# Optimization experiments

Hardware: AMD Instinct MI355X
Metric: run time of the kernel (lower is better)

Reference implementation:

```python
import jax, jax.numpy as jnp
import numpy as np

N_NODES = 50000
N_EDGES = 800000


def gat_layer(x, src, dst, W, al, ar, b, activation):
    # x: [N, F_in], W: [F_in, H*D], al/ar: [H, D], b: [H*D]
    H, D = al.shape
    n = x.shape[0]
    h = (x @ W).reshape(n, H, D)                      # [N, H, D]
    el = jnp.sum(h * al, axis=-1)                     # [N, H]
    er = jnp.sum(h * ar, axis=-1)                     # [N, H]
    e = jax.nn.leaky_relu(el[src] + er[dst], 0.2)     # [E, H]
    # segment softmax over incoming edges of each dst node
    m = jax.ops.segment_max(e, dst, num_segments=n)   # [N, H]
    ex = jnp.exp(e - m[dst])                          # [E, H]
    s = jax.ops.segment_sum(ex, dst, num_segments=n)  # [N, H]
    a = ex / s[dst]                                   # [E, H]
    msg = h[src] * a[:, :, None]                      # [E, H, D]
    out = jax.ops.segment_sum(msg, dst, num_segments=n) + b.reshape(1, H, D)
    return activation(out) if activation is not None else out


def setup_inputs() -> dict:
    key = jax.random.key(0)
    ks = jax.random.split(key, 12)
    feat = jax.random.normal(ks[0], (N_NODES, 128), dtype=jnp.float32)
    src = jax.random.randint(ks[1], (N_EDGES,), 0, N_NODES)
    dst = jax.random.randint(ks[2], (N_EDGES,), 0, N_NODES)
    sc = 0.1
    return {
        "feat": feat, "src": src, "dst": dst,
        "W1": jax.random.normal(ks[3], (128, 256), jnp.float32) * sc,
        "al1": jax.random.normal(ks[4], (4, 64), jnp.float32) * sc,
        "ar1": jax.random.normal(ks[5], (4, 64), jnp.float32) * sc,
        "b1": jnp.zeros((256,), jnp.float32),
        "W2": jax.random.normal(ks[6], (256, 256), jnp.float32) * sc,
        "al2": jax.random.normal(ks[7], (4, 64), jnp.float32) * sc,
        "ar2": jax.random.normal(ks[8], (4, 64), jnp.float32) * sc,
        "b2": jnp.zeros((256,), jnp.float32),
        "W3": jax.random.normal(ks[9], (256, 8), jnp.float32) * sc,
        "al3": jax.random.normal(ks[10], (1, 8), jnp.float32) * sc,
        "ar3": jax.random.normal(ks[11], (1, 8), jnp.float32) * sc,
        "b3": jnp.zeros((8,), jnp.float32),
    }


def reference(feat, src, dst, W1, al1, ar1, b1, W2, al2, ar2, b2, W3, al3, ar3, b3):
    n = feat.shape[0]
    elu = jax.nn.elu
    h = gat_layer(feat, src, dst, W1, al1, ar1, b1, elu).reshape(n, -1)  # flatten heads
    h = gat_layer(h, src, dst, W2, al2, ar2, b2, elu).reshape(n, -1)
    h = gat_layer(h, src, dst, W3, al3, ar3, b3, None)                   # [N, 1, out]
    return h.mean(axis=1)                                               # head mean -> [N, out]
```

## Files before the change

kernel.cpp:

```cpp
#include <hip/hip_runtime.h>
#include <math.h>


typedef _Float16 half8 __attribute__((ext_vector_type(8)));
typedef _Float16 half4 __attribute__((ext_vector_type(4)));
typedef float    floatx4 __attribute__((ext_vector_type(4)));

__device__ __forceinline__ float leaky02(float x) { return x > 0.f ? x : 0.2f * x; }

__global__ void count_edges(const int* __restrict__ dst, int* __restrict__ cnt, int E) {
    int i = blockIdx.x * blockDim.x + threadIdx.x;
    if (i < E) atomicAdd(&cnt[dst[i]], 1);
}

__global__ void scan_block(const int* __restrict__ cnt, int* __restrict__ incl,
                           int* __restrict__ bsum, int n) {
    __shared__ int sh[256];
    int tid = threadIdx.x;
    int i = blockIdx.x * 256 + tid;
    int v = (i < n) ? cnt[i] : 0;
    sh[tid] = v;
    __syncthreads();
    for (int o = 1; o < 256; o <<= 1) {
        int t = (tid >= o) ? sh[tid - o] : 0;
        __syncthreads();
        sh[tid] += t;
        __syncthreads();
    }
    if (i < n) incl[i] = sh[tid];
    if (tid == 255) bsum[blockIdx.x] = sh[255];
}

__global__ void scan_sums(int* __restrict__ bsum, int g) {
    __shared__ int sh[256];
    int tid = threadIdx.x;
    int v = (tid < g) ? bsum[tid] : 0;
    sh[tid] = v;
    __syncthreads();
    for (int o = 1; o < 256; o <<= 1) {
        int t = (tid >= o) ? sh[tid - o] : 0;
        __syncthreads();
        sh[tid] += t;
        __syncthreads();
    }
    if (tid < g) bsum[tid] = sh[tid] - v;
}

__global__ void finalize_rowptr(const int* __restrict__ incl, const int* __restrict__ cnt,
                                const int* __restrict__ bsum, int* __restrict__ row_ptr,
                                int* __restrict__ nxt, int n, int E) {
    int i = blockIdx.x * 256 + threadIdx.x;
    if (i < n) {
        int v = incl[i] - cnt[i] + bsum[blockIdx.x];
        row_ptr[i] = v;
        nxt[i] = v;
    }
    if (i == 0) row_ptr[n] = E;
}

__global__ void fill_csr(const int* __restrict__ src, const int* __restrict__ dst,
                         int* __restrict__ nxt, int* __restrict__ csr_src, int E) {
    int i = blockIdx.x * blockDim.x + threadIdx.x;
    if (i < E) {
        int p = atomicAdd(&nxt[dst[i]], 1);
        csr_src[p] = src[i];
    }
}

__global__ void transpose_w2(const float* __restrict__ W1, _Float16* __restrict__ W1T,
                             const float* __restrict__ W2, _Float16* __restrict__ W2T) {
    int i = blockIdx.x * 256 + threadIdx.x;
    if (i < 128 * 256) {
        int m = i >> 7, k = i & 127;
        W1T[i] = (_Float16)W1[k * 256 + m];
    } else {
        int j = i - 128 * 256;
        if (j < 256 * 256) {
            int m = j >> 8, k = j & 255;
            W2T[j] = (_Float16)W2[k * 256 + m];
        }
    }
}

#define GBM 128
#define GBK 32

template <bool AF32>
__global__ __launch_bounds__(256)
void gemm_mfma(const void* __restrict__ Ap, const _Float16* __restrict__ BT,
               _Float16* __restrict__ C, int N, int K) {
    __shared__ _Float16 As[GBM][GBK + 8];
    __shared__ _Float16 Bs[GBM][GBK + 8];
    int tid  = threadIdx.x;
    int wave = tid >> 6, lane = tid & 63;
    int quad = lane >> 4, l16 = lane & 15;
    int row0 = blockIdx.y * GBM;
    int col0 = blockIdx.x * GBM;

    floatx4 acc[8][2];
    #pragma unroll
    for (int i = 0; i < 8; ++i)
        #pragma unroll
        for (int j = 0; j < 2; ++j)
            #pragma unroll
            for (int e = 0; e < 4; ++e) acc[i][j][e] = 0.f;

    for (int k0 = 0; k0 < K; k0 += GBK) {
        if (AF32) {
            const float* Af = (const float*)Ap;
            #pragma unroll
            for (int it = 0; it < 4; ++it) {
                int s = it * 256 + tid;
                int r = s >> 3, off = (s & 7) * 4;
                float4 v = make_float4(0.f, 0.f, 0.f, 0.f);
                int gr = row0 + r;
                if (gr < N) v = *(const float4*)&Af[(size_t)gr * K + k0 + off];
                half4 hv;
                hv[0] = (_Float16)v.x; hv[1] = (_Float16)v.y;
                hv[2] = (_Float16)v.z; hv[3] = (_Float16)v.w;
                *(half4*)&As[r][off] = hv;
            }
        } else {
            const _Float16* Ah = (const _Float16*)Ap;
            #pragma unroll
            for (int it = 0; it < 2; ++it) {
                int s = it * 256 + tid;
                int r = s >> 2, off = (s & 3) * 8;
                half8 v;
                #pragma unroll
                for (int q = 0; q < 8; ++q) v[q] = (_Float16)0.f;
                int gr = row0 + r;
                if (gr < N) v = *(const half8*)&Ah[(size_t)gr * K + k0 + off];
                *(half8*)&As[r][off] = v;
            }
        }
        #pragma unroll
        for (int it = 0; it < 2; ++it) {
            int s = it * 256 + tid;
            int r = s >> 2, off = (s & 3) * 8;
            half8 w = *(const half8*)&BT[(size_t)(col0 + r) * K + k0 + off];
            *(half8*)&Bs[r][off] = w;
        }
        __syncthreads();
        half8 bfrag[2];
        #pragma unroll
        for (int ct = 0; ct < 2; ++ct)
            bfrag[ct] = *(const half8*)&Bs[wave * 32 + ct * 16 + l16][quad * 8];
        #pragma unroll
        for (int rt = 0; rt < 8; ++rt) {
            half8 afrag = *(const half8*)&As[rt * 16 + l16][quad * 8];
            acc[rt][0] = __builtin_amdgcn_mfma_f32_16x16x32_f16(afrag, bfrag[0], acc[rt][0], 0, 0, 0);
            acc[rt][1] = __builtin_amdgcn_mfma_f32_16x16x32_f16(afrag, bfrag[1], acc[rt][1], 0, 0, 0);
        }
        __syncthreads();
    }
    #pragma unroll
    for (int rt = 0; rt < 8; ++rt) {
        #pragma unroll
        for (int reg = 0; reg < 4; ++reg) {
            int gr = row0 + rt * 16 + quad * 4 + reg;
            if (gr < N) {
                #pragma unroll
                for (int ct = 0; ct < 2; ++ct) {
                    int gc = col0 + wave * 32 + ct * 16 + l16;
                    C[(size_t)gr * 256 + gc] = (_Float16)acc[rt][ct][reg];
                }
            }
        }
    }
}

__global__ __launch_bounds__(256)
void attn_lr(const _Float16* __restrict__ h16, const float* __restrict__ al,
             const float* __restrict__ ar, float* __restrict__ el,
             float* __restrict__ er, int NH) {
    int wid = (blockIdx.x * 256 + threadIdx.x) >> 6;
    int lane = threadIdx.x & 63;
    int r = lane >> 3, c = lane & 7;
    int row = wid * 8 + r;
    if (row >= NH) return;
    int hd = row & 3;
    half8 hv = *(const half8*)&h16[(size_t)row * 64 + c * 8];
    const float* alp = &al[hd * 64 + c * 8];
    const float* arp = &ar[hd * 64 + c * 8];
    float l = 0.f, rr = 0.f;
    #pragma unroll
    for (int q = 0; q < 8; ++q) {
        float v = (float)hv[q];
        l  += v * alp[q];
        rr += v * arp[q];
    }
    l  += __shfl_xor(l, 1);  l  += __shfl_xor(l, 2);  l  += __shfl_xor(l, 4);
    rr += __shfl_xor(rr, 1); rr += __shfl_xor(rr, 2); rr += __shfl_xor(rr, 4);
    if (c == 0) { el[row] = l; er[row] = rr; }
}

__global__ __launch_bounds__(256)
void gat_agg(const _Float16* __restrict__ h16, const float* __restrict__ el,
             const float* __restrict__ er, const int* __restrict__ row_ptr,
             const int* __restrict__ csr_src, const float* __restrict__ bias,
             _Float16* __restrict__ out, int N) {
    int tid = threadIdx.x;
    int l32 = tid & 31;
    int node = blockIdx.x * 8 + (tid >> 5);
    if (node >= N) return;
    int beg = row_ptr[node], end = row_ptr[node + 1];
    int deg = end - beg;
    int hd = l32 >> 3;

    float er0 = er[node * 4 + 0], er1 = er[node * 4 + 1];
    float er2 = er[node * 4 + 2], er3 = er[node * 4 + 3];

    float m0, m1, m2, m3, s0, s1, s2, s3;
    if (deg <= 32) {
        float e0 = -INFINITY, e1 = -INFINITY, e2 = -INFINITY, e3 = -INFINITY;
        bool act = l32 < deg;
        if (act) {
            int sv = csr_src[beg + l32];
            e0 = leaky02(el[sv * 4 + 0] + er0);
            e1 = leaky02(el[sv * 4 + 1] + er1);
            e2 = leaky02(el[sv * 4 + 2] + er2);
            e3 = leaky02(el[sv * 4 + 3] + er3);
        }
        m0 = e0; m1 = e1; m2 = e2; m3 = e3;
        #pragma unroll
        for (int msk = 1; msk < 32; msk <<= 1) {
            m0 = fmaxf(m0, __shfl_xor(m0, msk));
            m1 = fmaxf(m1, __shfl_xor(m1, msk));
            m2 = fmaxf(m2, __shfl_xor(m2, msk));
            m3 = fmaxf(m3, __shfl_xor(m3, msk));
        }
        s0 = act ? __expf(e0 - m0) : 0.f;
        s1 = act ? __expf(e1 - m1) : 0.f;
        s2 = act ? __expf(e2 - m2) : 0.f;
        s3 = act ? __expf(e3 - m3) : 0.f;
        #pragma unroll
        for (int msk = 1; msk < 32; msk <<= 1) {
            s0 += __shfl_xor(s0, msk);
            s1 += __shfl_xor(s1, msk);
            s2 += __shfl_xor(s2, msk);
            s3 += __shfl_xor(s3, msk);
        }
    } else {
        m0 = m1 = m2 = m3 = -INFINITY;
        for (int j = beg + l32; j < end; j += 32) {
            int sv = csr_src[j];
            m0 = fmaxf(m0, leaky02(el[sv * 4 + 0] + er0));
            m1 = fmaxf(m1, leaky02(el[sv * 4 + 1] + er1));
            m2 = fmaxf(m2, leaky02(el[sv * 4 + 2] + er2));
            m3 = fmaxf(m3, leaky02(el[sv * 4 + 3] + er3));
        }
        #pragma unroll
        for (int msk = 1; msk < 32; msk <<= 1) {
            m0 = fmaxf(m0, __shfl_xor(m0, msk));
            m1 = fmaxf(m1, __shfl_xor(m1, msk));
            m2 = fmaxf(m2, __shfl_xor(m2, msk));
            m3 = fmaxf(m3, __shfl_xor(m3, msk));
        }
        s0 = s1 = s2 = s3 = 0.f;
        for (int j = beg + l32; j < end; j += 32) {
            int sv = csr_src[j];
            s0 += __expf(leaky02(el[sv * 4 + 0] + er0) - m0);
            s1 += __expf(leaky02(el[sv * 4 + 1] + er1) - m1);
            s2 += __expf(leaky02(el[sv * 4 + 2] + er2) - m2);
            s3 += __expf(leaky02(el[sv * 4 + 3] + er3) - m3);
        }
        #pragma unroll
        for (int msk = 1; msk < 32; msk <<= 1) {
            s0 += __shfl_xor(s0, msk);
            s1 += __shfl_xor(s1, msk);
            s2 += __shfl_xor(s2, msk);
            s3 += __shfl_xor(s3, msk);
        }
    }
    float mh  = (hd & 2) ? ((hd & 1) ? m3 : m2) : ((hd & 1) ? m1 : m0);
    float sh_ = (hd & 2) ? ((hd & 1) ? s3 : s2) : ((hd & 1) ? s1 : s0);
    float erh = (hd & 2) ? ((hd & 1) ? er3 : er2) : ((hd & 1) ? er1 : er0);
    float ih  = sh_ > 0.f ? 1.f / sh_ : 0.f;

    const _Float16* hb = h16 + l32 * 8;
    float acc[8] = {};
    int j = beg;
    for (; j + 4 <= end; j += 4) {
        int sa = csr_src[j], sb = csr_src[j + 1], sc = csr_src[j + 2], sd = csr_src[j + 3];
        float wa = __expf(leaky02(el[sa * 4 + hd] + erh) - mh) * ih;
        float wb = __expf(leaky02(el[sb * 4 + hd] + erh) - mh) * ih;
        float wc = __expf(leaky02(el[sc * 4 + hd] + erh) - mh) * ih;
        float wd = __expf(leaky02(el[sd * 4 + hd] + erh) - mh) * ih;
        half8 va = *(const half8*)&hb[(size_t)sa * 256];
        half8 vb = *(const half8*)&hb[(size_t)sb * 256];
        half8 vc = *(const half8*)&hb[(size_t)sc * 256];
        half8 vd = *(const half8*)&hb[(size_t)sd * 256];
        #pragma unroll
        for (int q = 0; q < 8; ++q)
            acc[q] += wa * (float)va[q] + wb * (float)vb[q]
                    + wc * (float)vc[q] + wd * (float)vd[q];
    }
    for (; j < end; ++j) {
        int sv = csr_src[j];
        float w = __expf(leaky02(el[sv * 4 + hd] + erh) - mh) * ih;
        half8 v = *(const half8*)&hb[(size_t)sv * 256];
        #pragma unroll
        for (int q = 0; q < 8; ++q) acc[q] += w * (float)v[q];
    }
    half8 o;
    #pragma unroll
    for (int q = 0; q < 8; ++q) {
        float v = acc[q] + bias[l32 * 8 + q];
        v = v > 0.f ? v : (__expf(v) - 1.f);
        o[q] = (_Float16)v;
    }
    *(half8*)&out[(size_t)node * 256 + l32 * 8] = o;
}

__global__ __launch_bounds__(256)
void gemm3_attn(const _Float16* __restrict__ x, const float* __restrict__ W,
                const float* __restrict__ al, const float* __restrict__ ar,
                float* __restrict__ h3, float* __restrict__ el,
                float* __restrict__ er, int N) {
    __shared__ float Ws[256][9];
    int tid = threadIdx.x;
    #pragma unroll
    for (int d = 0; d < 8; ++d) Ws[tid][d] = W[tid * 8 + d];
    __syncthreads();
    int lane = tid & 63;
    int n = blockIdx.x * 4 + (tid >> 6);
    if (n >= N) return;
    float acc[8] = {};
    #pragma unroll
    for (int i = 0; i < 4; ++i) {
        int k = i * 64 + lane;
        float xv = (float)x[(size_t)n * 256 + k];
        #pragma unroll
        for (int d = 0; d < 8; ++d) acc[d] += xv * Ws[k][d];
    }
    #pragma unroll
    for (int d = 0; d < 8; ++d) {
        #pragma unroll
        for (int o = 32; o; o >>= 1) acc[d] += __shfl_down(acc[d], o);
    }
    if (lane == 0) {
        float l = 0.f, r = 0.f;
        #pragma unroll
        for (int d = 0; d < 8; ++d) {
            h3[n * 8 + d] = acc[d];
            l += acc[d] * al[d];
            r += acc[d] * ar[d];
        }
        el[n] = l;
        er[n] = r;
    }
}

__global__ __launch_bounds__(256)
void gat_agg3(const float* __restrict__ h3, const float* __restrict__ el,
              const float* __restrict__ er, const int* __restrict__ row_ptr,
              const int* __restrict__ csr_src, const float* __restrict__ bias,
              float* __restrict__ out, int N) {
    int tid = threadIdx.x;
    int lane = tid & 63;
    int n = blockIdx.x * 4 + (tid >> 6);
    if (n >= N) return;
    int beg = row_ptr[n], end = row_ptr[n + 1];
    float er_n = er[n];
    float mx = -INFINITY;
    for (int j = beg + lane; j < end; j += 64) {
        float e = leaky02(el[csr_src[j]] + er_n);
        mx = fmaxf(mx, e);
    }
    #pragma unroll
    for (int o = 1; o < 64; o <<= 1) mx = fmaxf(mx, __shfl_xor(mx, o));
    float sm = 0.f;
    for (int j = beg + lane; j < end; j += 64) {
        float e = leaky02(el[csr_src[j]] + er_n);
        sm += __expf(e - mx);
    }
    #pragma unroll
    for (int o = 1; o < 64; o <<= 1) sm += __shfl_xor(sm, o);
    float inv = sm > 0.f ? 1.0f / sm : 0.0f;
    int g = lane >> 3, c = lane & 7;
    float acc = 0.f;
    for (int j = beg + g; j < end; j += 8) {
        int s = csr_src[j];
        float a = __expf(leaky02(el[s] + er_n) - mx) * inv;
        acc += h3[s * 8 + c] * a;
    }
    acc += __shfl_xor(acc, 8);
    acc += __shfl_xor(acc, 16);
    acc += __shfl_xor(acc, 32);
    if (lane < 8) out[(size_t)n * 8 + lane] = acc + bias[lane];
}

static inline size_t align_up(size_t x, size_t a) { return (x + a - 1) & ~(a - 1); }

extern "C" void kernel_launch(void* const* d_in, const int* in_sizes, int n_in,
                              void* d_out, int out_size, void* d_ws, size_t ws_size,
                              hipStream_t stream) {
    const float* feat = (const float*)d_in[0];
    const int*   src  = (const int*)d_in[1];
    const int*   dst  = (const int*)d_in[2];
    const float* W1   = (const float*)d_in[3];
    const float* al1  = (const float*)d_in[4];
    const float* ar1  = (const float*)d_in[5];
    const float* b1   = (const float*)d_in[6];
    const float* W2   = (const float*)d_in[7];
    const float* al2  = (const float*)d_in[8];
    const float* ar2  = (const float*)d_in[9];
    const float* b2   = (const float*)d_in[10];
    const float* W3   = (const float*)d_in[11];
    const float* al3  = (const float*)d_in[12];
    const float* ar3  = (const float*)d_in[13];
    const float* b3   = (const float*)d_in[14];

    const int N = in_sizes[0] / 128;
    const int E = in_sizes[1];

    char* w = (char*)d_ws;
    _Float16* bufA16 = (_Float16*)w; w += align_up((size_t)N * 256 * 2, 256);
    _Float16* bufB16 = (_Float16*)w; w += align_up((size_t)N * 256 * 2, 256);
    _Float16* W1T    = (_Float16*)w; w += align_up((size_t)256 * 128 * 2, 256);
    _Float16* W2T    = (_Float16*)w; w += align_up((size_t)256 * 256 * 2, 256);
    float* el      = (float*)w; w += align_up((size_t)N * 4 * 4, 256);
    float* er      = (float*)w; w += align_up((size_t)N * 4 * 4, 256);
    float* h3      = (float*)w; w += align_up((size_t)N * 8 * 4, 256);
    int*   cnt     = (int*)w;   w += align_up((size_t)N * 4, 256);
    int*   incl    = (int*)w;   w += align_up((size_t)N * 4, 256);
    int*   bsum    = (int*)w;   w += align_up(256 * 4, 256);
    int*   row_ptr = (int*)w;   w += align_up(((size_t)N + 1) * 4, 256);
    int*   nxt     = (int*)w;   w += align_up((size_t)N * 4, 256);
    int*   csr_src = (int*)w;   w += align_up((size_t)E * 4, 256);
    (void)ws_size; (void)n_in; (void)out_size;

    const int G1 = (N + 255) / 256;
    const int GE = (E + 255) / 256;

    hipMemsetAsync(cnt, 0, (size_t)N * 4, stream);
    count_edges<<<GE, 256, 0, stream>>>(dst, cnt, E);
    scan_block<<<G1, 256, 0, stream>>>(cnt, incl, bsum, N);
    scan_sums<<<1, 256, 0, stream>>>(bsum, G1);
    finalize_rowptr<<<G1, 256, 0, stream>>>(incl, cnt, bsum, row_ptr, nxt, N, E);
    fill_csr<<<GE, 256, 0, stream>>>(src, dst, nxt, csr_src, E);

    transpose_w2<<<(128 * 256 + 256 * 256 + 255) / 256, 256, 0, stream>>>(W1, W1T, W2, W2T);

    dim3 ggrid(2, (N + GBM - 1) / GBM);
    const int GA = (N + 7) / 8;
    const int GL = (N * 4 + 31) / 32;

    gemm_mfma<true><<<ggrid, 256, 0, stream>>>(feat, W1T, bufA16, N, 128);
    attn_lr<<<GL, 256, 0, stream>>>(bufA16, al1, ar1, el, er, N * 4);
    gat_agg<<<GA, 256, 0, stream>>>(bufA16, el, er, row_ptr, csr_src, b1, bufB16, N);

    gemm_mfma<false><<<ggrid, 256, 0, stream>>>(bufB16, W2T, bufA16, N, 256);
    attn_lr<<<GL, 256, 0, stream>>>(bufA16, al2, ar2, el, er, N * 4);
    gat_agg<<<GA, 256, 0, stream>>>(bufA16, el, er, row_ptr, csr_src, b2, bufB16, N);

    gemm3_attn<<<(N + 3) / 4, 256, 0, stream>>>(bufB16, W3, al3, ar3, h3, el, er, N);
    gat_agg3<<<(N + 3) / 4, 256, 0, stream>>>(h3, el, er, row_ptr, csr_src, b3,
                                              (float*)d_out, N);
}
```

Measured before the change: 433.3 us.

## Fuse attention logits into GEMM epilogue and deepen aggregation gather unroll

Computes el/er attention logits directly from the MFMA accumulators in the GEMM epilogue, using shuffles and shared memory, which removes the separate attn_lr kernel and its reread of h. The scan_sums kernel is dropped and each finalize_rowptr block instead reduces the preceding block sums itself. gat_agg now uses float4 loads for el/er, preloads the bias, and unrolls the gather loop to 8 edges so more loads are in flight. The cost is extra GEMM epilogue work and higher register pressure in the aggregation kernel.

Result: slower. 463.6 us (+7.0%).

```diff
diff --git a/kernel.cpp b/kernel.cpp
--- a/kernel.cpp
+++ b/kernel.cpp
@@ -31,27 +31,23 @@
     if (tid == 255) bsum[blockIdx.x] = sh[255];
 }
 
-__global__ void scan_sums(int* __restrict__ bsum, int g) {
-    __shared__ int sh[256];
-    int tid = threadIdx.x;
-    int v = (tid < g) ? bsum[tid] : 0;
-    sh[tid] = v;
-    __syncthreads();
-    for (int o = 1; o < 256; o <<= 1) {
-        int t = (tid >= o) ? sh[tid - o] : 0;
-        __syncthreads();
-        sh[tid] += t;
-        __syncthreads();
-    }
-    if (tid < g) bsum[tid] = sh[tid] - v;
-}
-
 __global__ void finalize_rowptr(const int* __restrict__ incl, const int* __restrict__ cnt,
                                 const int* __restrict__ bsum, int* __restrict__ row_ptr,
                                 int* __restrict__ nxt, int n, int E) {
-    int i = blockIdx.x * 256 + threadIdx.x;
+    __shared__ int red[256];
+    int bid = blockIdx.x, tid = threadIdx.x;
+    int part = 0;
+    for (int i = tid; i < bid; i += 256) part += bsum[i];
+    red[tid] = part;
+    __syncthreads();
+    for (int o = 128; o; o >>= 1) {
+        if (tid < o) red[tid] += red[tid + o];
+        __syncthreads();
+    }
+    int base = red[0];
+    int i = bid * 256 + tid;
     if (i < n) {
-        int v = incl[i] - cnt[i] + bsum[blockIdx.x];
+        int v = incl[i] - cnt[i] + base;
         row_ptr[i] = v;
         nxt[i] = v;
     }
@@ -88,9 +84,13 @@
 template <bool AF32>
 __global__ __launch_bounds__(256)
 void gemm_mfma(const void* __restrict__ Ap, const _Float16* __restrict__ BT,
-               _Float16* __restrict__ C, int N, int K) {
+               const float* __restrict__ al, const float* __restrict__ ar,
+               _Float16* __restrict__ C, float* __restrict__ el,
+               float* __restrict__ er, int N, int K) {
     __shared__ _Float16 As[GBM][GBK + 8];
     __shared__ _Float16 Bs[GBM][GBK + 8];
+    __shared__ float shEl[4][GBM];
+    __shared__ float shEr[4][GBM];
     int tid  = threadIdx.x;
     int wave = tid >> 6, lane = tid & 63;
     int quad = lane >> 4, l16 = lane & 15;
@@ -154,6 +154,7 @@
         }
         __syncthreads();
     }
+
     #pragma unroll
     for (int rt = 0; rt < 8; ++rt) {
         #pragma unroll
@@ -168,31 +169,39 @@
             }
         }
     }
-}
-
-__global__ __launch_bounds__(256)
-void attn_lr(const _Float16* __restrict__ h16, const float* __restrict__ al,
-             const float* __restrict__ ar, float* __restrict__ el,
-             float* __restrict__ er, int NH) {
-    int wid = (blockIdx.x * 256 + threadIdx.x) >> 6;
-    int lane = threadIdx.x & 63;
-    int r = lane >> 3, c = lane & 7;
-    int row = wid * 8 + r;
-    if (row >= NH) return;
-    int hd = row & 3;
-    half8 hv = *(const half8*)&h16[(size_t)row * 64 + c * 8];
-    const float* alp = &al[hd * 64 + c * 8];
-    const float* arp = &ar[hd * 64 + c * 8];
-    float l = 0.f, rr = 0.f;
-    #pragma unroll
-    for (int q = 0; q < 8; ++q) {
-        float v = (float)hv[q];
-        l  += v * alp[q];
-        rr += v * arp[q];
-    }
-    l  += __shfl_xor(l, 1);  l  += __shfl_xor(l, 2);  l  += __shfl_xor(l, 4);
-    rr += __shfl_xor(rr, 1); rr += __shfl_xor(rr, 2); rr += __shfl_xor(rr, 4);
-    if (c == 0) { el[row] = l; er[row] = rr; }
+
+    int hw = (col0 >> 6) + (wave >> 1);
+    int doff = ((wave & 1) * 32) + l16;
+    float al0 = al[hw * 64 + doff], al1 = al[hw * 64 + doff + 16];
+    float ar0 = ar[hw * 64 + doff], ar1 = ar[hw * 64 + doff + 16];
+    #pragma unroll
+    for (int rt = 0; rt < 8; ++rt) {
+        #pragma unroll
+        for (int reg = 0; reg < 4; ++reg) {
+            float e_l = acc[rt][0][reg] * al0 + acc[rt][1][reg] * al1;
+            float e_r = acc[rt][0][reg] * ar0 + acc[rt][1][reg] * ar1;
+            #pragma unroll
+            for (int m = 1; m <= 8; m <<= 1) {
+                e_l += __shfl_xor(e_l, m);
+                e_r += __shfl_xor(e_r, m);
+            }
+            if (l16 == 0) {
+                int row = rt * 16 + quad * 4 + reg;
+                shEl[wave][row] = e_l;
+                shEr[wave][row] = e_r;
+            }
+        }
+    }
+    __syncthreads();
+    {
+        int row = tid & 127, p = tid >> 7;
+        int gr = row0 + row;
+        if (gr < N) {
+            int head = (col0 >> 6) + p;
+            el[(size_t)gr * 4 + head] = shEl[2 * p][row] + shEl[2 * p + 1][row];
+            er[(size_t)gr * 4 + head] = shEr[2 * p][row] + shEr[2 * p + 1][row];
+        }
+    }
 }
 
 __global__ __launch_bounds__(256)
@@ -208,8 +217,11 @@
     int deg = end - beg;
     int hd = l32 >> 3;
 
-    float er0 = er[node * 4 + 0], er1 = er[node * 4 + 1];
-    float er2 = er[node * 4 + 2], er3 = er[node * 4 + 3];
+    float4 ern4 = *(const float4*)&er[node * 4];
+    float er0 = ern4.x, er1 = ern4.y, er2 = ern4.z, er3 = ern4.w;
+    float bsv[8];
+    #pragma unroll
+    for (int q = 0; q < 8; ++q) bsv[q] = bias[l32 * 8 + q];
 
     float m0, m1, m2, m3, s0, s1, s2, s3;
     if (deg <= 32) {
@@ -217,10 +229,11 @@
         bool act = l32 < deg;
         if (act) {
             int sv = csr_src[beg + l32];
-            e0 = leaky02(el[sv * 4 + 0] + er0);
-            e1 = leaky02(el[sv * 4 + 1] + er1);
-            e2 = leaky02(el[sv * 4 + 2] + er2);
-            e3 = leaky02(el[sv * 4 + 3] + er3);
+            float4 elv = *(const float4*)&el[sv * 4];
+            e0 = leaky02(elv.x + er0);
+            e1 = leaky02(elv.y + er1);
+            e2 = leaky02(elv.z + er2);
+            e3 = leaky02(elv.w + er3);
         }
         m0 = e0; m1 = e1; m2 = e2; m3 = e3;
         #pragma unroll
@@ -245,10 +258,11 @@
         m0 = m1 = m2 = m3 = -INFINITY;
         for (int j = beg + l32; j < end; j += 32) {
             int sv = csr_src[j];
-            m0 = fmaxf(m0, leaky02(el[sv * 4 + 0] + er0));
-            m1 = fmaxf(m1, leaky02(el[sv * 4 + 1] + er1));
-            m2 = fmaxf(m2, leaky02(el[sv * 4 + 2] + er2));
-            m3 = fmaxf(m3, leaky02(el[sv * 4 + 3] + er3));
+            float4 elv = *(const float4*)&el[sv * 4];
+            m0 = fmaxf(m0, leaky02(elv.x + er0));
+            m1 = fmaxf(m1, leaky02(elv.y + er1));
+            m2 = fmaxf(m2, leaky02(elv.z + er2));
+            m3 = fmaxf(m3, leaky02(elv.w + er3));
         }
         #pragma unroll
         for (int msk = 1; msk < 32; msk <<= 1) {
@@ -260,10 +274,11 @@
         s0 = s1 = s2 = s3 = 0.f;
         for (int j = beg + l32; j < end; j += 32) {
             int sv = csr_src[j];
-            s0 += __expf(leaky02(el[sv * 4 + 0] + er0) - m0);
-            s1 += __expf(leaky02(el[sv * 4 + 1] + er1) - m1);
-            s2 += __expf(leaky02(el[sv * 4 + 2] + er2) - m2);
-            s3 += __expf(leaky02(el[sv * 4 + 3] + er3) - m3);
+            float4 elv = *(const float4*)&el[sv * 4];
+            s0 += __expf(leaky02(elv.x + er0) - m0);
+            s1 += __expf(leaky02(elv.y + er1) - m1);
+            s2 += __expf(leaky02(elv.z + er2) - m2);
+            s3 += __expf(leaky02(elv.w + er3) - m3);
         }
         #pragma unroll
         for (int msk = 1; msk < 32; msk <<= 1) {
@@ -281,20 +296,21 @@
     const _Float16* hb = h16 + l32 * 8;
     float acc[8] = {};
     int j = beg;
-    for (; j + 4 <= end; j += 4) {
-        int sa = csr_src[j], sb = csr_src[j + 1], sc = csr_src[j + 2], sd = csr_src[j + 3];
-        float wa = __expf(leaky02(el[sa * 4 + hd] + erh) - mh) * ih;
-        float wb = __expf(leaky02(el[sb * 4 + hd] + erh) - mh) * ih;
-        float wc = __expf(leaky02(el[sc * 4 + hd] + erh) - mh) * ih;
-        float wd = __expf(leaky02(el[sd * 4 + hd] + erh) - mh) * ih;
-        half8 va = *(const half8*)&hb[(size_t)sa * 256];
-        half8 vb = *(const half8*)&hb[(size_t)sb * 256];
-        half8 vc = *(const half8*)&hb[(size_t)sc * 256];
-        half8 vd = *(const half8*)&hb[(size_t)sd * 256];
-        #pragma unroll
-        for (int q = 0; q < 8; ++q)
-            acc[q] += wa * (float)va[q] + wb * (float)vb[q]
-                    + wc * (float)vc[q] + wd * (float)vd[q];
+    for (; j + 8 <= end; j += 8) {
+        int   se[8];
+        float we[8];
+        half8 ve[8];
+        #pragma unroll
+        for (int u = 0; u < 8; ++u) se[u] = csr_src[j + u];
+        #pragma unroll
+        for (int u = 0; u < 8; ++u) ve[u] = *(const half8*)&hb[(size_t)se[u] * 256];
+        #pragma unroll
+        for (int u = 0; u < 8; ++u)
+            we[u] = __expf(leaky02(el[se[u] * 4 + hd] + erh) - mh) * ih;
+        #pragma unroll
+        for (int u = 0; u < 8; ++u)
+            #pragma unroll
+            for (int q = 0; q < 8; ++q) acc[q] += we[u] * (float)ve[u][q];
     }
     for (; j < end; ++j) {
         int sv = csr_src[j];
@@ -306,7 +322,7 @@
     half8 o;
     #pragma unroll
     for (int q = 0; q < 8; ++q) {
-        float v = acc[q] + bias[l32 * 8 + q];
+        float v = acc[q] + bsv[q];
         v = v > 0.f ? v : (__expf(v) - 1.f);
         o[q] = (_Float16)v;
     }
@@ -437,7 +453,6 @@
     hipMemsetAsync(cnt, 0, (size_t)N * 4, stream);
     count_edges<<<GE, 256, 0, stream>>>(dst, cnt, E);
     scan_block<<<G1, 256, 0, stream>>>(cnt, incl, bsum, N);
-    scan_sums<<<1, 256, 0, stream>>>(bsum, G1);
     finalize_rowptr<<<G1, 256, 0, stream>>>(incl, cnt, bsum, row_ptr, nxt, N, E);
     fill_csr<<<GE, 256, 0, stream>>>(src, dst, nxt, csr_src, E);
 
@@ -445,14 +460,11 @@
 
     dim3 ggrid(2, (N + GBM - 1) / GBM);
     const int GA = (N + 7) / 8;
-    const int GL = (N * 4 + 31) / 32;
-
-    gemm_mfma<true><<<ggrid, 256, 0, stream>>>(feat, W1T, bufA16, N, 128);
-    attn_lr<<<GL, 256, 0, stream>>>(bufA16, al1, ar1, el, er, N * 4);
+
+    gemm_mfma<true><<<ggrid, 256, 0, stream>>>(feat, W1T, al1, ar1, bufA16, el, er, N, 128);
     gat_agg<<<GA, 256, 0, stream>>>(bufA16, el, er, row_ptr, csr_src, b1, bufB16, N);
 
-    gemm_mfma<false><<<ggrid, 256, 0, stream>>>(bufB16, W2T, bufA16, N, 256);
-    attn_lr<<<GL, 256, 0, stream>>>(bufA16, al2, ar2, el, er, N * 4);
+    gemm_mfma<false><<<ggrid, 256, 0, stream>>>(bufB16, W2T, al2, ar2, bufA16, el, er, N, 256);
     gat_agg<<<GA, 256, 0, stream>>>(bufA16, el, er, row_ptr, csr_src, b2, bufB16, N);
 
     gemm3_attn<<<(N + 3) / 4, 256, 0, stream>>>(bufB16, W3, al3, ar3, h3, el, er, N);
```

## Cache softmax weights in LDS for low-degree nodes and fold block-sum scan into finalize

Applied to the files above, without the earlier changes.

For nodes with at most 32 incoming edges, gat_agg now computes the normalized attention weights once per edge and stores them with the source indices in shared memory. The aggregation loop then reads these back instead of reloading csr_src and el and recomputing exp for every lane. el/er loads are vectorized as float4. The separate scan_sums launch is removed; each finalize_rowptr block instead reduces the preceding block sums itself, which trades one kernel launch for redundant reduction work.

New measurement: 430.6 us. No clear change (-0.6%).

```diff
diff --git a/kernel.cpp b/kernel.cpp
--- a/kernel.cpp
+++ b/kernel.cpp
@@ -31,27 +31,23 @@
     if (tid == 255) bsum[blockIdx.x] = sh[255];
 }
 
-__global__ void scan_sums(int* __restrict__ bsum, int g) {
-    __shared__ int sh[256];
-    int tid = threadIdx.x;
-    int v = (tid < g) ? bsum[tid] : 0;
-    sh[tid] = v;
-    __syncthreads();
-    for (int o = 1; o < 256; o <<= 1) {
-        int t = (tid >= o) ? sh[tid - o] : 0;
-        __syncthreads();
-        sh[tid] += t;
-        __syncthreads();
-    }
-    if (tid < g) bsum[tid] = sh[tid] - v;
-}
-
 __global__ void finalize_rowptr(const int* __restrict__ incl, const int* __restrict__ cnt,
                                 const int* __restrict__ bsum, int* __restrict__ row_ptr,
                                 int* __restrict__ nxt, int n, int E) {
-    int i = blockIdx.x * 256 + threadIdx.x;
+    __shared__ int red[256];
+    int bid = blockIdx.x, tid = threadIdx.x;
+    int part = 0;
+    for (int i = tid; i < bid; i += 256) part += bsum[i];
+    red[tid] = part;
+    __syncthreads();
+    for (int o = 128; o; o >>= 1) {
+        if (tid < o) red[tid] += red[tid + o];
+        __syncthreads();
+    }
+    int base = red[0];
+    int i = bid * 256 + tid;
     if (i < n) {
-        int v = incl[i] - cnt[i] + bsum[blockIdx.x];
+        int v = incl[i] - cnt[i] + base;
         row_ptr[i] = v;
         nxt[i] = v;
     }
@@ -200,29 +196,36 @@
              const float* __restrict__ er, const int* __restrict__ row_ptr,
              const int* __restrict__ csr_src, const float* __restrict__ bias,
              _Float16* __restrict__ out, int N) {
+    __shared__ int   sbuf[8][32];
+    __shared__ float wbuf[8][32][4];
     int tid = threadIdx.x;
     int l32 = tid & 31;
-    int node = blockIdx.x * 8 + (tid >> 5);
+    int g = tid >> 5;
+    int node = blockIdx.x * 8 + g;
     if (node >= N) return;
     int beg = row_ptr[node], end = row_ptr[node + 1];
     int deg = end - beg;
     int hd = l32 >> 3;
 
-    float er0 = er[node * 4 + 0], er1 = er[node * 4 + 1];
-    float er2 = er[node * 4 + 2], er3 = er[node * 4 + 3];
-
-    float m0, m1, m2, m3, s0, s1, s2, s3;
+    float4 ern4 = *(const float4*)&er[node * 4];
+    float er0 = ern4.x, er1 = ern4.y, er2 = ern4.z, er3 = ern4.w;
+
+    const _Float16* hb = h16 + l32 * 8;
+    float acc[8] = {};
+
     if (deg <= 32) {
+        bool act = l32 < deg;
+        int sv = 0;
         float e0 = -INFINITY, e1 = -INFINITY, e2 = -INFINITY, e3 = -INFINITY;
-        bool act = l32 < deg;
         if (act) {
-            int sv = csr_src[beg + l32];
-            e0 = leaky02(el[sv * 4 + 0] + er0);
-            e1 = leaky02(el[sv * 4 + 1] + er1);
-            e2 = leaky02(el[sv * 4 + 2] + er2);
-            e3 = leaky02(el[sv * 4 + 3] + er3);
-        }
-        m0 = e0; m1 = e1; m2 = e2; m3 = e3;
+            sv = csr_src[beg + l32];
+            float4 elv = *(const float4*)&el[sv * 4];
+            e0 = leaky02(elv.x + er0);
+            e1 = leaky02(elv.y + er1);
+            e2 = leaky02(elv.z + er2);
+            e3 = leaky02(elv.w + er3);
+        }
+        float m0 = e0, m1 = e1, m2 = e2, m3 = e3;
         #pragma unroll
         for (int msk = 1; msk < 32; msk <<= 1) {
             m0 = fmaxf(m0, __shfl_xor(m0, msk));
@@ -230,10 +233,11 @@
             m2 = fmaxf(m2, __shfl_xor(m2, msk));
             m3 = fmaxf(m3, __shfl_xor(m3, msk));
         }
-        s0 = act ? __expf(e0 - m0) : 0.f;
-        s1 = act ? __expf(e1 - m1) : 0.f;
-        s2 = act ? __expf(e2 - m2) : 0.f;
-        s3 = act ? __expf(e3 - m3) : 0.f;
+        float x0 = act ? __expf(e0 - m0) : 0.f;
+        float x1 = act ? __expf(e1 - m1) : 0.f;
+        float x2 = act ? __expf(e2 - m2) : 0.f;
+        float x3 = act ? __expf(e3 - m3) : 0.f;
+        float s0 = x0, s1 = x1, s2 = x2, s3 = x3;
         #pragma unroll
         for (int msk = 1; msk < 32; msk <<= 1) {
             s0 += __shfl_xor(s0, msk);
@@ -241,14 +245,48 @@
             s2 += __shfl_xor(s2, msk);
             s3 += __shfl_xor(s3, msk);
         }
+        float i0 = s0 > 0.f ? 1.f / s0 : 0.f;
+        float i1 = s1 > 0.f ? 1.f / s1 : 0.f;
+        float i2 = s2 > 0.f ? 1.f / s2 : 0.f;
+        float i3 = s3 > 0.f ? 1.f / s3 : 0.f;
+        if (act) {
+            sbuf[g][l32] = sv;
+            wbuf[g][l32][0] = x0 * i0;
+            wbuf[g][l32][1] = x1 * i1;
+            wbuf[g][l32][2] = x2 * i2;
+            wbuf[g][l32][3] = x3 * i3;
+        }
+        int t = 0;
+        for (; t + 4 <= deg; t += 4) {
+            int sa = sbuf[g][t],     sb = sbuf[g][t + 1];
+            int sc = sbuf[g][t + 2], sd = sbuf[g][t + 3];
+            float wa = wbuf[g][t][hd],     wb = wbuf[g][t + 1][hd];
+            float wc = wbuf[g][t + 2][hd], wd = wbuf[g][t + 3][hd];
+            half8 va = *(const half8*)&hb[(size_t)sa * 256];
+            half8 vb = *(const half8*)&hb[(size_t)sb * 256];
+            half8 vc = *(const half8*)&hb[(size_t)sc * 256];
+            half8 vd = *(const half8*)&hb[(size_t)sd * 256];
+            #pragma unroll
+            for (int q = 0; q < 8; ++q)
+                acc[q] += wa * (float)va[q] + wb * (float)vb[q]
+                        + wc * (float)vc[q] + wd * (float)vd[q];
+        }
+        for (; t < deg; ++t) {
+            int s = sbuf[g][t];
+            float w = wbuf[g][t][hd];
+            half8 v = *(const half8*)&hb[(size_t)s * 256];
+            #pragma unroll
+            for (int q = 0; q < 8; ++q) acc[q] += w * (float)v[q];
+        }
     } else {
-        m0 = m1 = m2 = m3 = -INFINITY;
+        float m0 = -INFINITY, m1 = -INFINITY, m2 = -INFINITY, m3 = -INFINITY;
         for (int j = beg + l32; j < end; j += 32) {
             int sv = csr_src[j];
-            m0 = fmaxf(m0, leaky02(el[sv * 4 + 0] + er0));
-            m1 = fmaxf(m1, leaky02(el[sv * 4 + 1] + er1));
-            m2 = fmaxf(m2, leaky02(el[sv * 4 + 2] + er2));
-            m3 = fmaxf(m3, leaky02(el[sv * 4 + 3] + er3));
+            float4 elv = *(const float4*)&el[sv * 4];
+            m0 = fmaxf(m0, leaky02(elv.x + er0));
+            m1 = fmaxf(m1, leaky02(elv.y + er1));
+            m2 = fmaxf(m2, leaky02(elv.z + er2));
+            m3 = fmaxf(m3, leaky02(elv.w + er3));
         }
         #pragma unroll
         for (int msk = 1; msk < 32; msk <<= 1) {
@@ -257,13 +295,14 @@
             m2 = fmaxf(m2, __shfl_xor(m2, msk));
             m3 = fmaxf(m3, __shfl_xor(m3, msk));
         }
-        s0 = s1 = s2 = s3 = 0.f;
+        float s0 = 0.f, s1 = 0.f, s2 = 0.f, s3 = 0.f;
         for (int j = beg + l32; j < end; j += 32) {
             int sv = csr_src[j];
-            s0 += __expf(leaky02(el[sv * 4 + 0] + er0) - m0);
-            s1 += __expf(leaky02(el[sv * 4 + 1] + er1) - m1);
-            s2 += __expf(leaky02(el[sv * 4 + 2] + er2) - m2);
-            s3 += __expf(leaky02(el[sv * 4 + 3] + er3) - m3);
+            float4 elv = *(const float4*)&el[sv * 4];
+            s0 += __expf(leaky02(elv.x + er0) - m0);
+            s1 += __expf(leaky02(elv.y + er1) - m1);
+            s2 += __expf(leaky02(elv.z + er2) - m2);
+            s3 += __expf(leaky02(elv.w + er3) - m3);
         }
         #pragma unroll
         for (int msk = 1; msk < 32; msk <<= 1) {
@@ -272,37 +311,35 @@
             s2 += __shfl_xor(s2, msk);
             s3 += __shfl_xor(s3, msk);
         }
-    }
-    float mh  = (hd & 2) ? ((hd & 1) ? m3 : m2) : ((hd & 1) ? m1 : m0);
-    float sh_ = (hd & 2) ? ((hd & 1) ? s3 : s2) : ((hd & 1) ? s1 : s0);
-    float erh = (hd & 2) ? ((hd & 1) ? er3 : er2) : ((hd & 1) ? er1 : er0);
-    float ih  = sh_ > 0.f ? 1.f / sh_ : 0.f;
-
-    const _Float16* hb = h16 + l32 * 8;
-    float acc[8] = {};
-    int j = beg;
-    for (; j + 4 <= end; j += 4) {
-        int sa = csr_src[j], sb = csr_src[j + 1], sc = csr_src[j + 2], sd = csr_src[j + 3];
-        float wa = __expf(leaky02(el[sa * 4 + hd] + erh) - mh) * ih;
-        float wb = __expf(leaky02(el[sb * 4 + hd] + erh) - mh) * ih;
-        float wc = __expf(leaky02(el[sc * 4 + hd] + erh) - mh) * ih;
-        float wd = __expf(leaky02(el[sd * 4 + hd] + erh) - mh) * ih;
-        half8 va = *(const half8*)&hb[(size_t)sa * 256];
-        half8 vb = *(const half8*)&hb[(size_t)sb * 256];
-        half8 vc = *(const half8*)&hb[(size_t)sc * 256];
-        half8 vd = *(const half8*)&hb[(size_t)sd * 256];
-        #pragma unroll
-        for (int q = 0; q < 8; ++q)
-            acc[q] += wa * (float)va[q] + wb * (float)vb[q]
-                    + wc * (float)vc[q] + wd * (float)vd[q];
-    }
-    for (; j < end; ++j) {
-        int sv = csr_src[j];
-        float w = __expf(leaky02(el[sv * 4 + hd] + erh) - mh) * ih;
-        half8 v = *(const half8*)&hb[(size_t)sv * 256];
-        #pragma unroll
-        for (int q = 0; q < 8; ++q) acc[q] += w * (float)v[q];
-    }
+        float mh  = (hd & 2) ? ((hd & 1) ? m3 : m2) : ((hd & 1) ? m1 : m0);
+        float sh_ = (hd & 2) ? ((hd & 1) ? s3 : s2) : ((hd & 1) ? s1 : s0);
+        float erh = (hd & 2) ? ((hd & 1) ? er3 : er2) : ((hd & 1) ? er1 : er0);
+        float ih  = sh_ > 0.f ? 1.f / sh_ : 0.f;
+        int j = beg;
+        for (; j + 4 <= end; j += 4) {
+            int sa = csr_src[j], sb = csr_src[j + 1], sc = csr_src[j + 2], sd = csr_src[j + 3];
+            float wa = __expf(leaky02(el[sa * 4 + hd] + erh) - mh) * ih;
+            float wb = __expf(leaky02(el[sb * 4 + hd] + erh) - mh) * ih;
+            float wc = __expf(leaky02(el[sc * 4 + hd] + erh) - mh) * ih;
+            float wd = __expf(leaky02(el[sd * 4 + hd] + erh) - mh) * ih;
+            half8 va = *(const half8*)&hb[(size_t)sa * 256];
+            half8 vb = *(const half8*)&hb[(size_t)sb * 256];
+            half8 vc = *(const half8*)&hb[(size_t)sc * 256];
+            half8 vd = *(const half8*)&hb[(size_t)sd * 256];
+            #pragma unroll
+            for (int q = 0; q < 8; ++q)
+                acc[q] += wa * (float)va[q] + wb * (float)vb[q]
+                        + wc * (float)vc[q] + wd * (float)vd[q];
+        }
+        for (; j < end; ++j) {
+            int sv = csr_src[j];
+            float w = __expf(leaky02(el[sv * 4 + hd] + erh) - mh) * ih;
+            half8 v = *(const half8*)&hb[(size_t)sv * 256];
+            #pragma unroll
+            for (int q = 0; q < 8; ++q) acc[q] += w * (float)v[q];
+        }
+    }
+
     half8 o;
     #pragma unroll
     for (int q = 0; q < 8; ++q) {
@@ -437,7 +474,6 @@
     hipMemsetAsync(cnt, 0, (size_t)N * 4, stream);
     count_edges<<<GE, 256, 0, stream>>>(dst, cnt, E);
     scan_block<<<G1, 256, 0, stream>>>(cnt, incl, bsum, N);
-    scan_sums<<<1, 256, 0, stream>>>(bsum, G1);
     finalize_rowptr<<<G1, 256, 0, stream>>>(incl, cnt, bsum, row_ptr, nxt, N, E);
     fill_csr<<<GE, 256, 0, stream>>>(src, dst, nxt, csr_src, E);
 
```
